# Performance work log

Hardware: AMD Instinct MI355X
Metric: run time of the kernel (lower is better)

The kernel has to match this reference:

```python
import jax, jax.numpy as jnp
import numpy as np

T, B, I, H, NC = 1024, 256, 128, 64, 10


def _lstm_cell(x_t, h, c, W_ih, W_hh, b):
    # PyTorch gate order: i, f, g, o. gates: [B, 4H]
    gates = x_t @ W_ih.T + h @ W_hh.T + b
    i, f, g, o = jnp.split(gates, 4, axis=-1)
    i = jax.nn.sigmoid(i)
    f = jax.nn.sigmoid(f)
    g = jnp.tanh(g)
    o = jax.nn.sigmoid(o)
    c = f * c + i * g
    h = o * jnp.tanh(c)
    return h, c


def setup_inputs() -> dict:
    key = jax.random.key(0)
    ks = jax.random.split(key, 12)
    s = 1.0 / np.sqrt(H)  # PyTorch LSTM init scale
    d = {
        "x": jax.random.normal(ks[0], (T, B, I), dtype=jnp.float32),
        # forward direction LSTM params
        "W_ih_f": jax.random.uniform(ks[1], (4 * H, I), minval=-s, maxval=s, dtype=jnp.float32),
        "W_hh_f": jax.random.uniform(ks[2], (4 * H, H), minval=-s, maxval=s, dtype=jnp.float32),
        "b_f": jax.random.uniform(ks[3], (4 * H,), minval=-s, maxval=s, dtype=jnp.float32),
        # reverse direction LSTM params
        "W_ih_r": jax.random.uniform(ks[4], (4 * H, I), minval=-s, maxval=s, dtype=jnp.float32),
        "W_hh_r": jax.random.uniform(ks[5], (4 * H, H), minval=-s, maxval=s, dtype=jnp.float32),
        "b_r": jax.random.uniform(ks[6], (4 * H,), minval=-s, maxval=s, dtype=jnp.float32),
        # MLP head: 2H -> 64 -> 32 -> NC
        "fc1_w": jax.random.normal(ks[7], (64, 2 * H), dtype=jnp.float32) * 0.05,
        "fc1_b": jnp.zeros((64,), dtype=jnp.float32),
        "fc2_w": jax.random.normal(ks[8], (32, 64), dtype=jnp.float32) * 0.05,
        "fc2_b": jnp.zeros((32,), dtype=jnp.float32),
        "fc3_w": jax.random.normal(ks[9], (NC, 32), dtype=jnp.float32) * 0.05,
        "fc3_b": jnp.zeros((NC,), dtype=jnp.float32),
    }
    return d


def _forward(x, W_ih_f, W_hh_f, b_f, W_ih_r, W_hh_r, b_r,
             fc1_w, fc1_b, fc2_w, fc2_b, fc3_w, fc3_b):
    Bsz = x.shape[1]
    h0 = jnp.zeros((Bsz, H), dtype=x.dtype)
    c0 = jnp.zeros((Bsz, H), dtype=x.dtype)

    # Forward direction: only the final hidden state is needed (output[-1] fwd half).
    def fwd_step(carry, x_t):
        h, c = carry
        h, c = _lstm_cell(x_t, h, c, W_ih_f, W_hh_f, b_f)
        return (h, c), None

    (h_fwd_last, _), _ = jax.lax.scan(fwd_step, (h0, c0), x)

    # Reverse direction: output[-1] reverse half is the hidden after processing
    # x[-1] first (reverse scan starts from the last timestep with zero state).
    h_bwd_last, _ = _lstm_cell(x[-1], h0, c0, W_ih_r, W_hh_r, b_r)

    h_cat = jnp.concatenate([h_fwd_last, h_bwd_last], axis=-1)  # [B, 2H]

    h1 = jax.nn.relu(h_cat @ fc1_w.T + fc1_b)
    h2 = jax.nn.relu(h1 @ fc2_w.T + fc2_b)
    out = h2 @ fc3_w.T + fc3_b  # [B, NC]
    return out


def reference(x, W_ih_f, W_hh_f, b_f, W_ih_r, W_hh_r, b_r,
              fc1_w, fc1_b, fc2_w, fc2_b, fc3_w, fc3_b):
    return _forward(x, W_ih_f, W_hh_f, b_f, W_ih_r, W_hh_r, b_r,
                    fc1_w, fc1_b, fc2_w, fc2_b, fc3_w, fc3_b)
```

## Files before the change

kernel.cpp:

```cpp
#include <hip/hip_runtime.h>
#include <math.h>

#define T_LEN 1024
#define B_SZ  256
#define I_SZ  128
#define H_SZ  64
#define G_SZ  256
#define SUB   32

typedef float f32x8 __attribute__((ext_vector_type(8)));
typedef float f32x2 __attribute__((ext_vector_type(2)));

__device__ __forceinline__ float fast_tanh(float x) {
    float e = __expf(-2.0f * fabsf(x));
    float r = (1.0f - e) * __builtin_amdgcn_rcpf(1.0f + e);
    return copysignf(r, x);
}

#define LD8PIN(V, P)                                                        \
    {   float4 t0_ = *reinterpret_cast<const float4*>(P);                   \
        float4 t1_ = *reinterpret_cast<const float4*>((P) + 4);             \
        V = (f32x8){t0_.x, t0_.y, t0_.z, t0_.w, t1_.x, t1_.y, t1_.z, t1_.w};\
        asm volatile("" : "+v"(V)); }

#define RL16(VA, VB, K)                                                     \
    {   unsigned s0_  = __builtin_amdgcn_readlane(hu, (K) + 0);             \
        unsigned s1_  = __builtin_amdgcn_readlane(hu, (K) + 1);             \
        unsigned s2_  = __builtin_amdgcn_readlane(hu, (K) + 2);             \
        unsigned s3_  = __builtin_amdgcn_readlane(hu, (K) + 3);             \
        unsigned s4_  = __builtin_amdgcn_readlane(hu, (K) + 4);             \
        unsigned s5_  = __builtin_amdgcn_readlane(hu, (K) + 5);             \
        unsigned s6_  = __builtin_amdgcn_readlane(hu, (K) + 6);             \
        unsigned s7_  = __builtin_amdgcn_readlane(hu, (K) + 7);             \
        unsigned s8_  = __builtin_amdgcn_readlane(hu, (K) + 8);             \
        unsigned s9_  = __builtin_amdgcn_readlane(hu, (K) + 9);             \
        unsigned s10_ = __builtin_amdgcn_readlane(hu, (K) + 10);            \
        unsigned s11_ = __builtin_amdgcn_readlane(hu, (K) + 11);            \
        unsigned s12_ = __builtin_amdgcn_readlane(hu, (K) + 12);            \
        unsigned s13_ = __builtin_amdgcn_readlane(hu, (K) + 13);            \
        unsigned s14_ = __builtin_amdgcn_readlane(hu, (K) + 14);            \
        unsigned s15_ = __builtin_amdgcn_readlane(hu, (K) + 15);            \
        a0 = fmaf(__uint_as_float(s0_),  VA[0], a0);                        \
        a1 = fmaf(__uint_as_float(s1_),  VA[1], a1);                        \
        a2 = fmaf(__uint_as_float(s2_),  VA[2], a2);                        \
        a3 = fmaf(__uint_as_float(s3_),  VA[3], a3);                        \
        a0 = fmaf(__uint_as_float(s4_),  VA[4], a0);                        \
        a1 = fmaf(__uint_as_float(s5_),  VA[5], a1);                        \
        a2 = fmaf(__uint_as_float(s6_),  VA[6], a2);                        \
        a3 = fmaf(__uint_as_float(s7_),  VA[7], a3);                        \
        a0 = fmaf(__uint_as_float(s8_),  VB[0], a0);                        \
        a1 = fmaf(__uint_as_float(s9_),  VB[1], a1);                        \
        a2 = fmaf(__uint_as_float(s10_), VB[2], a2);                        \
        a3 = fmaf(__uint_as_float(s11_), VB[3], a3);                        \
        a0 = fmaf(__uint_as_float(s12_), VB[4], a0);                        \
        a1 = fmaf(__uint_as_float(s13_), VB[5], a1);                        \
        a2 = fmaf(__uint_as_float(s14_), VB[6], a2);                        \
        a3 = fmaf(__uint_as_float(s15_), VB[7], a3); }

__device__ __forceinline__ int swz(int c) { return c + 4 * (c >> 5); }

#define GLOAD(K0)                                                           \
    { _Pragma("unroll") for (int i_ = 0; i_ < 4; ++i_) {                    \
        const int mr_ = srow + 32 * i_;                                     \
        pa[i_] = *reinterpret_cast<const float4*>(                          \
            &xch[(size_t)(mt * 128 + mr_) * I_SZ + (K0) + skk]);            \
        pb[i_] = *reinterpret_cast<const float4*>(                          \
            &W_ih[(size_t)(nt * 128 + mr_) * I_SZ + (K0) + skk]); } }

#define SWRITE(BUF)                                                         \
    { _Pragma("unroll") for (int i_ = 0; i_ < 4; ++i_) {                    \
        const int mr_ = srow + 32 * i_; const int sm_ = swz(mr_);           \
        as[BUF][skk + 0][sm_] = pa[i_].x; as[BUF][skk + 1][sm_] = pa[i_].y; \
        as[BUF][skk + 2][sm_] = pa[i_].z; as[BUF][skk + 3][sm_] = pa[i_].w; \
        bs[BUF][skk + 0][sm_] = pb[i_].x; bs[BUF][skk + 1][sm_] = pb[i_].y; \
        bs[BUF][skk + 2][sm_] = pb[i_].z; bs[BUF][skk + 3][sm_] = pb[i_].w; } }

__global__ __launch_bounds__(256, 2) void xg_gemm(
    const float* __restrict__ xch,
    const float* __restrict__ W_ih,
    const float* __restrict__ bias,
    float* __restrict__ XG)
{
    const int tid = threadIdx.x;
    const int tx  = tid & 15;
    const int ty  = tid >> 4;
    const int mt  = blockIdx.x;
    const int nt  = blockIdx.y;

    __shared__ __align__(16) float as[2][32][140];
    __shared__ __align__(16) float bs[2][32][140];

    const int n0 = nt * 128 + tx * 8;
    float4 bia = *reinterpret_cast<const float4*>(&bias[n0]);
    float4 bib = *reinterpret_cast<const float4*>(&bias[n0 + 4]);

    f32x2 acc2[8][4];
#pragma unroll
    for (int r = 0; r < 8; ++r)
#pragma unroll
        for (int cc = 0; cc < 4; ++cc) acc2[r][cc] = (f32x2){0.0f, 0.0f};

    const int srow = tid >> 3;
    const int skk  = (tid & 7) * 4;

    float4 pa[4], pb[4];
    GLOAD(0) SWRITE(0)
    __syncthreads();

#pragma unroll
    for (int ks = 0; ks < 4; ++ks) {
        if (ks < 3) GLOAD((ks + 1) * 32)

        const int buf = ks & 1;
#pragma unroll 8
        for (int kk = 0; kk < 32; ++kk) {
            const float4 a0 = *reinterpret_cast<const float4*>(&as[buf][kk][swz(ty * 8)]);
            const float4 a1 = *reinterpret_cast<const float4*>(&as[buf][kk][swz(ty * 8) + 4]);
            const float4 b0 = *reinterpret_cast<const float4*>(&bs[buf][kk][swz(tx * 8)]);
            const float4 b1 = *reinterpret_cast<const float4*>(&bs[buf][kk][swz(tx * 8) + 4]);
            const float av[8] = {a0.x, a0.y, a0.z, a0.w, a1.x, a1.y, a1.z, a1.w};
            const f32x2 bv2[4] = {{b0.x, b0.y}, {b0.z, b0.w},
                                  {b1.x, b1.y}, {b1.z, b1.w}};
#pragma unroll
            for (int r = 0; r < 8; ++r) {
                const f32x2 a2 = {av[r], av[r]};
#pragma unroll
                for (int cc = 0; cc < 4; ++cc)
                    acc2[r][cc] = a2 * bv2[cc] + acc2[r][cc];
            }
        }

        if (ks < 3) {
            SWRITE(buf ^ 1)
            __syncthreads();
        }
    }

#pragma unroll
    for (int r = 0; r < 8; ++r) {
        const size_t m = (size_t)(mt * 128 + ty * 8 + r);
        float4 o0 = {acc2[r][0].x + bia.x, acc2[r][0].y + bia.y,
                     acc2[r][1].x + bia.z, acc2[r][1].y + bia.w};
        float4 o1 = {acc2[r][2].x + bib.x, acc2[r][2].y + bib.y,
                     acc2[r][3].x + bib.z, acc2[r][3].y + bib.w};
        *reinterpret_cast<float4*>(&XG[m * G_SZ + n0])     = o0;
        *reinterpret_cast<float4*>(&XG[m * G_SZ + n0 + 4]) = o1;
    }
}

__global__ __launch_bounds__(256, 1) void lstm_rec(
    const float* __restrict__ XG,
    const float* __restrict__ W_hh,
    float* __restrict__ h_state,
    float* __restrict__ c_state,
    int TC, int first)
{
    const int b = blockIdx.x;
    const int t = threadIdx.x;
    const int l = t & 63;
    const int g = t >> 6;
    const int row = t;

    __shared__ __align__(16) float xgl[2][SUB][G_SZ];
    __shared__ float gs[2][G_SZ];

    const float* ur = W_hh + row * H_SZ;
    f32x8 w0, w1, w2, w3, w4, w5, w6, w7;
    LD8PIN(w0, ur)      LD8PIN(w1, ur +  8) LD8PIN(w2, ur + 16) LD8PIN(w3, ur + 24)
    LD8PIN(w4, ur + 32) LD8PIN(w5, ur + 40) LD8PIN(w6, ur + 48) LD8PIN(w7, ur + 56)

    float h = first ? 0.0f : h_state[b * H_SZ + l];
    float c = first ? 0.0f : c_state[b * H_SZ + l];

    {
        float* xf = &xgl[0][0][0];
#pragma unroll
        for (int i = 0; i < 8; ++i) {
            const int F = t + 256 * i;
            const int r = F >> 6, cw = F & 63;
            *reinterpret_cast<float4*>(xf + 4 * F) =
                *reinterpret_cast<const float4*>(
                    XG + ((size_t)r * B_SZ + b) * G_SZ + 4 * cw);
        }
    }
    __syncthreads();

    const bool isg = (g == 2);
    const int nsub = TC / SUB;
    int db = 0;

    for (int sub = 0; sub < nsub; ++sub) {
        const int cur = sub & 1;
        if (sub + 1 < nsub) {
            float* xf = &xgl[cur ^ 1][0][0];
#pragma unroll
            for (int i = 0; i < 8; ++i) {
                const int F = t + 256 * i;
                const int r = (F >> 6) + (sub + 1) * SUB, cw = F & 63;
                *reinterpret_cast<float4*>(xf + 4 * F) =
                    *reinterpret_cast<const float4*>(
                        XG + ((size_t)r * B_SZ + b) * G_SZ + 4 * cw);
            }
        }

#pragma unroll 4
        for (int ts = 0; ts < SUB; ++ts) {
            const unsigned hu = __float_as_uint(h);
            float a0 = xgl[cur][ts][row];
            float a1 = 0.0f, a2 = 0.0f, a3 = 0.0f;
            RL16(w0, w1,  0) RL16(w2, w3, 16)
            RL16(w4, w5, 32) RL16(w6, w7, 48)
            const float acc = (a0 + a1) + (a2 + a3);

            const float arg = isg ? (-2.0f * acc) : (-acc);
            const float e = __expf(arg);
            const float r = __builtin_amdgcn_rcpf(1.0f + e);
            const float a = isg ? (1.0f - e) * r : r;

            gs[db][row] = a;
            __syncthreads();

            const float ig = gs[db][l];
            const float fg = gs[db][H_SZ + l];
            const float gg = gs[db][2 * H_SZ + l];
            const float og = gs[db][3 * H_SZ + l];
            c = fmaf(fg, c, ig * gg);
            h = og * fast_tanh(c);
            db ^= 1;
        }
    }

    if (t < H_SZ) {
        h_state[b * H_SZ + t] = h;
        c_state[b * H_SZ + t] = c;
    }
}

__global__ __launch_bounds__(256, 1) void lstm_tail(
    const float* __restrict__ x_last,
    const float* __restrict__ W_ih_r,
    const float* __restrict__ b_r,
    const float* __restrict__ h_fwd,
    const float* __restrict__ fc1_w,
    const float* __restrict__ fc1_b,
    const float* __restrict__ fc2_w,
    const float* __restrict__ fc2_b,
    const float* __restrict__ fc3_w,
    const float* __restrict__ fc3_b,
    float* __restrict__ out)
{
    const int b = blockIdx.x;
    const int j = threadIdx.x;

    __shared__ float xs[I_SZ];
    __shared__ float gs[G_SZ];
    __shared__ float hc[2 * H_SZ];
    __shared__ float h1[64];
    __shared__ float h2[32];

    if (j < I_SZ) xs[j] = x_last[(size_t)b * I_SZ + j];
    if (j < H_SZ) hc[j] = h_fwd[b * H_SZ + j];
    __syncthreads();

    float a0 = b_r[j], a1 = 0.0f, a2 = 0.0f, a3 = 0.0f;
    const float* wrow = W_ih_r + j * I_SZ;
#pragma unroll
    for (int kk = 0; kk < I_SZ; kk += 4) {
        float4 wv = *reinterpret_cast<const float4*>(wrow + kk);
        a0 = fmaf(xs[kk + 0], wv.x, a0);
        a1 = fmaf(xs[kk + 1], wv.y, a1);
        a2 = fmaf(xs[kk + 2], wv.z, a2);
        a3 = fmaf(xs[kk + 3], wv.w, a3);
    }
    const float acc = (a0 + a1) + (a2 + a3);
    const int gate = j >> 6;
    gs[j] = (gate == 2) ? tanhf(acc) : 1.0f / (1.0f + expf(-acc));
    __syncthreads();

    if (j < H_SZ) {
        const float cc = gs[j] * gs[2 * H_SZ + j];
        hc[H_SZ + j] = gs[3 * H_SZ + j] * tanhf(cc);
    }
    __syncthreads();

    if (j < 64) {
        float s0 = fc1_b[j], s1 = 0.0f, s2 = 0.0f, s3 = 0.0f;
        const float* w = fc1_w + j * 128;
#pragma unroll
        for (int kk = 0; kk < 128; kk += 4) {
            float4 wv = *reinterpret_cast<const float4*>(w + kk);
            s0 = fmaf(hc[kk + 0], wv.x, s0);
            s1 = fmaf(hc[kk + 1], wv.y, s1);
            s2 = fmaf(hc[kk + 2], wv.z, s2);
            s3 = fmaf(hc[kk + 3], wv.w, s3);
        }
        h1[j] = fmaxf((s0 + s1) + (s2 + s3), 0.0f);
    }
    __syncthreads();

    if (j < 32) {
        float s0 = fc2_b[j], s1 = 0.0f, s2 = 0.0f, s3 = 0.0f;
        const float* w = fc2_w + j * 64;
#pragma unroll
        for (int kk = 0; kk < 64; kk += 4) {
            float4 wv = *reinterpret_cast<const float4*>(w + kk);
            s0 = fmaf(h1[kk + 0], wv.x, s0);
            s1 = fmaf(h1[kk + 1], wv.y, s1);
            s2 = fmaf(h1[kk + 2], wv.z, s2);
            s3 = fmaf(h1[kk + 3], wv.w, s3);
        }
        h2[j] = fmaxf((s0 + s1) + (s2 + s3), 0.0f);
    }
    __syncthreads();

    if (j < 10) {
        float s = fc3_b[j];
#pragma unroll
        for (int kk = 0; kk < 32; ++kk) s = fmaf(h2[kk], fc3_w[j * 32 + kk], s);
        out[b * 10 + j] = s;
    }
}

extern "C" void kernel_launch(void* const* d_in, const int* in_sizes, int n_in,
                              void* d_out, int out_size, void* d_ws, size_t ws_size,
                              hipStream_t stream) {
    const float* x      = (const float*)d_in[0];
    const float* W_ih_f = (const float*)d_in[1];
    const float* W_hh_f = (const float*)d_in[2];
    const float* b_f    = (const float*)d_in[3];
    const float* W_ih_r = (const float*)d_in[4];
    const float* b_r    = (const float*)d_in[6];
    const float* fc1_w  = (const float*)d_in[7];
    const float* fc1_b  = (const float*)d_in[8];
    const float* fc2_w  = (const float*)d_in[9];
    const float* fc2_b  = (const float*)d_in[10];
    const float* fc3_w  = (const float*)d_in[11];
    const float* fc3_b  = (const float*)d_in[12];
    float* out = (float*)d_out;

    int TC = 1024;
    while (TC > 64 &&
           (size_t)TC * B_SZ * G_SZ * 4 + 2 * B_SZ * H_SZ * 4 > ws_size)
        TC >>= 1;

    float* XG      = (float*)d_ws;
    float* h_state = (float*)((char*)d_ws + (size_t)TC * B_SZ * G_SZ * 4);
    float* c_state = h_state + B_SZ * H_SZ;

    const int NCH = T_LEN / TC;
    for (int ch = 0; ch < NCH; ++ch) {
        const float* xch = x + (size_t)ch * TC * B_SZ * I_SZ;
        hipLaunchKernelGGL(xg_gemm, dim3(TC * B_SZ / 128, 2), dim3(256), 0,
                           stream, xch, W_ih_f, b_f, XG);
        hipLaunchKernelGGL(lstm_rec, dim3(B_SZ), dim3(256), 0, stream,
                           XG, W_hh_f, h_state, c_state, TC, ch == 0 ? 1 : 0);
    }

    const float* x_last = x + (size_t)(T_LEN - 1) * B_SZ * I_SZ;
    hipLaunchKernelGGL(lstm_tail, dim3(B_SZ), dim3(256), 0, stream,
                       x_last, W_ih_r, b_r, h_state,
                       fc1_w, fc1_b, fc2_w, fc2_b, fc3_w, fc3_b, out);
}
```

Before: 606.9 us.

## Overlap next-chunk input GEMM with current-chunk recurrence in one fused launch

Merges the input-projection GEMM and the LSTM recurrence into a single kernel. Each launch runs 256 recurrence blocks for the current time chunk plus extra GEMM blocks that compute the next chunk's gate inputs into a second, double-buffered workspace. The GEMM work is meant to hide behind the latency-bound recurrence, which leaves most CUs idle. In exchange the chunk shrinks to 256 steps, so there are more launches and state reloads, and the GEMM blocks may contend with recurrence blocks for CU resources.

```diff
diff --git a/kernel.cpp b/kernel.cpp
--- a/kernel.cpp
+++ b/kernel.cpp
@@ -75,164 +75,167 @@
         bs[BUF][skk + 0][sm_] = pb[i_].x; bs[BUF][skk + 1][sm_] = pb[i_].y; \
         bs[BUF][skk + 2][sm_] = pb[i_].z; bs[BUF][skk + 3][sm_] = pb[i_].w; } }
 
-__global__ __launch_bounds__(256, 2) void xg_gemm(
+__global__ __launch_bounds__(256, 1) void rec_gemm(
+    const float* __restrict__ XGin,
+    const float* __restrict__ W_hh,
+    float* __restrict__ h_state,
+    float* __restrict__ c_state,
+    int TC, int first, int nrec,
     const float* __restrict__ xch,
     const float* __restrict__ W_ih,
     const float* __restrict__ bias,
-    float* __restrict__ XG)
+    float* __restrict__ XGout,
+    int MT)
 {
-    const int tid = threadIdx.x;
-    const int tx  = tid & 15;
-    const int ty  = tid >> 4;
-    const int mt  = blockIdx.x;
-    const int nt  = blockIdx.y;
-
-    __shared__ __align__(16) float as[2][32][140];
-    __shared__ __align__(16) float bs[2][32][140];
-
-    const int n0 = nt * 128 + tx * 8;
-    float4 bia = *reinterpret_cast<const float4*>(&bias[n0]);
-    float4 bib = *reinterpret_cast<const float4*>(&bias[n0 + 4]);
-
-    f32x2 acc2[8][4];
-#pragma unroll
-    for (int r = 0; r < 8; ++r)
-#pragma unroll
-        for (int cc = 0; cc < 4; ++cc) acc2[r][cc] = (f32x2){0.0f, 0.0f};
-
-    const int srow = tid >> 3;
-    const int skk  = (tid & 7) * 4;
-
-    float4 pa[4], pb[4];
-    GLOAD(0) SWRITE(0)
-    __syncthreads();
-
-#pragma unroll
-    for (int ks = 0; ks < 4; ++ks) {
-        if (ks < 3) GLOAD((ks + 1) * 32)
-
-        const int buf = ks & 1;
-#pragma unroll 8
-        for (int kk = 0; kk < 32; ++kk) {
-            const float4 a0 = *reinterpret_cast<const float4*>(&as[buf][kk][swz(ty * 8)]);
-            const float4 a1 = *reinterpret_cast<const float4*>(&as[buf][kk][swz(ty * 8) + 4]);
-            const float4 b0 = *reinterpret_cast<const float4*>(&bs[buf][kk][swz(tx * 8)]);
-            const float4 b1 = *reinterpret_cast<const float4*>(&bs[buf][kk][swz(tx * 8) + 4]);
-            const float av[8] = {a0.x, a0.y, a0.z, a0.w, a1.x, a1.y, a1.z, a1.w};
-            const f32x2 bv2[4] = {{b0.x, b0.y}, {b0.z, b0.w},
-                                  {b1.x, b1.y}, {b1.z, b1.w}};
-#pragma unroll
-            for (int r = 0; r < 8; ++r) {
-                const f32x2 a2 = {av[r], av[r]};
-#pragma unroll
-                for (int cc = 0; cc < 4; ++cc)
-                    acc2[r][cc] = a2 * bv2[cc] + acc2[r][cc];
-            }
-        }
-
-        if (ks < 3) {
-            SWRITE(buf ^ 1)
-            __syncthreads();
-        }
-    }
-
-#pragma unroll
-    for (int r = 0; r < 8; ++r) {
-        const size_t m = (size_t)(mt * 128 + ty * 8 + r);
-        float4 o0 = {acc2[r][0].x + bia.x, acc2[r][0].y + bia.y,
-                     acc2[r][1].x + bia.z, acc2[r][1].y + bia.w};
-        float4 o1 = {acc2[r][2].x + bib.x, acc2[r][2].y + bib.y,
-                     acc2[r][3].x + bib.z, acc2[r][3].y + bib.w};
-        *reinterpret_cast<float4*>(&XG[m * G_SZ + n0])     = o0;
-        *reinterpret_cast<float4*>(&XG[m * G_SZ + n0 + 4]) = o1;
-    }
-}
-
-__global__ __launch_bounds__(256, 1) void lstm_rec(
-    const float* __restrict__ XG,
-    const float* __restrict__ W_hh,
-    float* __restrict__ h_state,
-    float* __restrict__ c_state,
-    int TC, int first)
-{
-    const int b = blockIdx.x;
-    const int t = threadIdx.x;
-    const int l = t & 63;
-    const int g = t >> 6;
-    const int row = t;
-
-    __shared__ __align__(16) float xgl[2][SUB][G_SZ];
-    __shared__ float gs[2][G_SZ];
-
-    const float* ur = W_hh + row * H_SZ;
-    f32x8 w0, w1, w2, w3, w4, w5, w6, w7;
-    LD8PIN(w0, ur)      LD8PIN(w1, ur +  8) LD8PIN(w2, ur + 16) LD8PIN(w3, ur + 24)
-    LD8PIN(w4, ur + 32) LD8PIN(w5, ur + 40) LD8PIN(w6, ur + 48) LD8PIN(w7, ur + 56)
-
-    float h = first ? 0.0f : h_state[b * H_SZ + l];
-    float c = first ? 0.0f : c_state[b * H_SZ + l];
-
-    {
-        float* xf = &xgl[0][0][0];
-#pragma unroll
-        for (int i = 0; i < 8; ++i) {
-            const int F = t + 256 * i;
-            const int r = F >> 6, cw = F & 63;
-            *reinterpret_cast<float4*>(xf + 4 * F) =
-                *reinterpret_cast<const float4*>(
-                    XG + ((size_t)r * B_SZ + b) * G_SZ + 4 * cw);
-        }
-    }
-    __syncthreads();
-
-    const bool isg = (g == 2);
-    const int nsub = TC / SUB;
-    int db = 0;
-
-    for (int sub = 0; sub < nsub; ++sub) {
-        const int cur = sub & 1;
-        if (sub + 1 < nsub) {
-            float* xf = &xgl[cur ^ 1][0][0];
+    __shared__ __align__(16) float smem[17920];
+
+    if ((int)blockIdx.x < nrec) {
+        float (*xgl)[SUB][G_SZ] = reinterpret_cast<float(*)[SUB][G_SZ]>(smem);
+        float (*gs)[G_SZ]       = reinterpret_cast<float(*)[G_SZ]>(smem + 16384);
+
+        const int b = blockIdx.x;
+        const int t = threadIdx.x;
+        const int l = t & 63;
+        const int g = t >> 6;
+        const int row = t;
+
+        const float* ur = W_hh + row * H_SZ;
+        f32x8 w0, w1, w2, w3, w4, w5, w6, w7;
+        LD8PIN(w0, ur)      LD8PIN(w1, ur +  8) LD8PIN(w2, ur + 16) LD8PIN(w3, ur + 24)
+        LD8PIN(w4, ur + 32) LD8PIN(w5, ur + 40) LD8PIN(w6, ur + 48) LD8PIN(w7, ur + 56)
+
+        float h = first ? 0.0f : h_state[b * H_SZ + l];
+        float c = first ? 0.0f : c_state[b * H_SZ + l];
+
+        {
+            float* xf = &xgl[0][0][0];
 #pragma unroll
             for (int i = 0; i < 8; ++i) {
                 const int F = t + 256 * i;
-                const int r = (F >> 6) + (sub + 1) * SUB, cw = F & 63;
+                const int r = F >> 6, cw = F & 63;
                 *reinterpret_cast<float4*>(xf + 4 * F) =
                     *reinterpret_cast<const float4*>(
-                        XG + ((size_t)r * B_SZ + b) * G_SZ + 4 * cw);
-            }
-        }
+                        XGin + ((size_t)r * B_SZ + b) * G_SZ + 4 * cw);
+            }
+        }
+        __syncthreads();
+
+        const bool isg = (g == 2);
+        const int nsub = TC / SUB;
+        int db = 0;
+
+        for (int sub = 0; sub < nsub; ++sub) {
+            const int cur = sub & 1;
+            if (sub + 1 < nsub) {
+                float* xf = &xgl[cur ^ 1][0][0];
+#pragma unroll
+                for (int i = 0; i < 8; ++i) {
+                    const int F = t + 256 * i;
+                    const int r = (F >> 6) + (sub + 1) * SUB, cw = F & 63;
+                    *reinterpret_cast<float4*>(xf + 4 * F) =
+                        *reinterpret_cast<const float4*>(
+                            XGin + ((size_t)r * B_SZ + b) * G_SZ + 4 * cw);
+                }
+            }
 
 #pragma unroll 4
-        for (int ts = 0; ts < SUB; ++ts) {
-            const unsigned hu = __float_as_uint(h);
-            float a0 = xgl[cur][ts][row];
-            float a1 = 0.0f, a2 = 0.0f, a3 = 0.0f;
-            RL16(w0, w1,  0) RL16(w2, w3, 16)
-            RL16(w4, w5, 32) RL16(w6, w7, 48)
-            const float acc = (a0 + a1) + (a2 + a3);
-
-            const float arg = isg ? (-2.0f * acc) : (-acc);
-            const float e = __expf(arg);
-            const float r = __builtin_amdgcn_rcpf(1.0f + e);
-            const float a = isg ? (1.0f - e) * r : r;
-
-            gs[db][row] = a;
-            __syncthreads();
-
-            const float ig = gs[db][l];
-            const float fg = gs[db][H_SZ + l];
-            const float gg = gs[db][2 * H_SZ + l];
-            const float og = gs[db][3 * H_SZ + l];
-            c = fmaf(fg, c, ig * gg);
-            h = og * fast_tanh(c);
-            db ^= 1;
-        }
-    }
-
-    if (t < H_SZ) {
-        h_state[b * H_SZ + t] = h;
-        c_state[b * H_SZ + t] = c;
+            for (int ts = 0; ts < SUB; ++ts) {
+                const unsigned hu = __float_as_uint(h);
+                float a0 = xgl[cur][ts][row];
+                float a1 = 0.0f, a2 = 0.0f, a3 = 0.0f;
+                RL16(w0, w1,  0) RL16(w2, w3, 16)
+                RL16(w4, w5, 32) RL16(w6, w7, 48)
+                const float acc = (a0 + a1) + (a2 + a3);
+
+                const float arg = isg ? (-2.0f * acc) : (-acc);
+                const float e = __expf(arg);
+                const float r = __builtin_amdgcn_rcpf(1.0f + e);
+                const float a = isg ? (1.0f - e) * r : r;
+
+                gs[db][row] = a;
+                __syncthreads();
+
+                const float ig = gs[db][l];
+                const float fg = gs[db][H_SZ + l];
+                const float gg = gs[db][2 * H_SZ + l];
+                const float og = gs[db][3 * H_SZ + l];
+                c = fmaf(fg, c, ig * gg);
+                h = og * fast_tanh(c);
+                db ^= 1;
+            }
+        }
+
+        if (t < H_SZ) {
+            h_state[b * H_SZ + t] = h;
+            c_state[b * H_SZ + t] = c;
+        }
+    } else {
+        float (*as)[32][140] = reinterpret_cast<float(*)[32][140]>(smem);
+        float (*bs)[32][140] = reinterpret_cast<float(*)[32][140]>(smem + 8960);
+
+        const int gb  = blockIdx.x - nrec;
+        const int mt  = gb % MT;
+        const int nt  = gb / MT;
+        const int tid = threadIdx.x;
+        const int tx  = tid & 15;
+        const int ty  = tid >> 4;
+
+        const int n0 = nt * 128 + tx * 8;
+        float4 bia = *reinterpret_cast<const float4*>(&bias[n0]);
+        float4 bib = *reinterpret_cast<const float4*>(&bias[n0 + 4]);
+
+        f32x2 acc2[8][4];
+#pragma unroll
+        for (int r = 0; r < 8; ++r)
+#pragma unroll
+            for (int cc = 0; cc < 4; ++cc) acc2[r][cc] = (f32x2){0.0f, 0.0f};
+
+        const int srow = tid >> 3;
+        const int skk  = (tid & 7) * 4;
+
+        float4 pa[4], pb[4];
+        GLOAD(0) SWRITE(0)
+        __syncthreads();
+
+#pragma unroll
+        for (int ks = 0; ks < 4; ++ks) {
+            if (ks < 3) GLOAD((ks + 1) * 32)
+
+            const int buf = ks & 1;
+#pragma unroll 8
+            for (int kk = 0; kk < 32; ++kk) {
+                const float4 a0 = *reinterpret_cast<const float4*>(&as[buf][kk][swz(ty * 8)]);
+                const float4 a1 = *reinterpret_cast<const float4*>(&as[buf][kk][swz(ty * 8) + 4]);
+                const float4 b0 = *reinterpret_cast<const float4*>(&bs[buf][kk][swz(tx * 8)]);
+                const float4 b1 = *reinterpret_cast<const float4*>(&bs[buf][kk][swz(tx * 8) + 4]);
+                const float av[8] = {a0.x, a0.y, a0.z, a0.w, a1.x, a1.y, a1.z, a1.w};
+                const f32x2 bv2[4] = {{b0.x, b0.y}, {b0.z, b0.w},
+                                      {b1.x, b1.y}, {b1.z, b1.w}};
+#pragma unroll
+                for (int r = 0; r < 8; ++r) {
+                    const f32x2 a2 = {av[r], av[r]};
+#pragma unroll
+                    for (int cc = 0; cc < 4; ++cc)
+                        acc2[r][cc] = a2 * bv2[cc] + acc2[r][cc];
+                }
+            }
+
+            if (ks < 3) {
+                SWRITE(buf ^ 1)
+                __syncthreads();
+            }
+        }
+
+#pragma unroll
+        for (int r = 0; r < 8; ++r) {
+            const size_t m = (size_t)(mt * 128 + ty * 8 + r);
+            float4 o0 = {acc2[r][0].x + bia.x, acc2[r][0].y + bia.y,
+                         acc2[r][1].x + bia.z, acc2[r][1].y + bia.w};
+            float4 o1 = {acc2[r][2].x + bib.x, acc2[r][2].y + bib.y,
+                         acc2[r][3].x + bib.z, acc2[r][3].y + bib.w};
+            *reinterpret_cast<float4*>(&XGout[m * G_SZ + n0])     = o0;
+            *reinterpret_cast<float4*>(&XGout[m * G_SZ + n0 + 4]) = o1;
+        }
     }
 }
 
@@ -338,22 +341,34 @@
     const float* fc3_b  = (const float*)d_in[12];
     float* out = (float*)d_out;
 
-    int TC = 1024;
+    int TC = 256;
     while (TC > 64 &&
-           (size_t)TC * B_SZ * G_SZ * 4 + 2 * B_SZ * H_SZ * 4 > ws_size)
+           2 * (size_t)TC * B_SZ * G_SZ * 4 + 2 * B_SZ * H_SZ * 4 > ws_size)
         TC >>= 1;
 
-    float* XG      = (float*)d_ws;
-    float* h_state = (float*)((char*)d_ws + (size_t)TC * B_SZ * G_SZ * 4);
+    const size_t xg_elems = (size_t)TC * B_SZ * G_SZ;
+    float* XGbuf[2];
+    XGbuf[0] = (float*)d_ws;
+    XGbuf[1] = XGbuf[0] + xg_elems;
+    float* h_state = XGbuf[1] + xg_elems;
     float* c_state = h_state + B_SZ * H_SZ;
 
     const int NCH = T_LEN / TC;
+    const int MT  = TC * B_SZ / 128;
+
+    hipLaunchKernelGGL(rec_gemm, dim3(2 * MT), dim3(256), 0, stream,
+                       XGbuf[0], W_hh_f, h_state, c_state, TC, 1, 0,
+                       x, W_ih_f, b_f, XGbuf[0], MT);
+
     for (int ch = 0; ch < NCH; ++ch) {
-        const float* xch = x + (size_t)ch * TC * B_SZ * I_SZ;
-        hipLaunchKernelGGL(xg_gemm, dim3(TC * B_SZ / 128, 2), dim3(256), 0,
-                           stream, xch, W_ih_f, b_f, XG);
-        hipLaunchKernelGGL(lstm_rec, dim3(B_SZ), dim3(256), 0, stream,
-                           XG, W_hh_f, h_state, c_state, TC, ch == 0 ? 1 : 0);
+        const bool hasg = (ch + 1 < NCH);
+        const float* xnext = hasg ? x + (size_t)(ch + 1) * TC * B_SZ * I_SZ : x;
+        float* XGout = XGbuf[(ch + 1) & 1];
+        const int grid = B_SZ + (hasg ? 2 * MT : 0);
+        hipLaunchKernelGGL(rec_gemm, dim3(grid), dim3(256), 0, stream,
+                           XGbuf[ch & 1], W_hh_f, h_state, c_state,
+                           TC, ch == 0 ? 1 : 0, B_SZ,
+                           xnext, W_ih_f, b_f, XGout, MT);
     }
 
     const float* x_last = x + (size_t)(T_LEN - 1) * B_SZ * I_SZ;
```

New measurement: 694.1 us. 14.4% more time.
